# Kernel optimization log

Hardware: AMD Instinct MI355X
Metric: run time of the kernel (lower is better)

The kernel has to match this reference:

```python
import jax, jax.numpy as jnp
import numpy as np
from jax import lax

NPOINT = 1024
RADIUS = 0.2
NSAMPLE = 32
BN_EPS = 1e-5


def fps(xyz, npoint):
    """Deterministic farthest point sampling (start index 0). xyz: (B,N,3) -> (B,npoint) int32."""
    B, N, _ = xyz.shape

    def step(carry, _):
        distance, farthest = carry
        centroid = jnp.take_along_axis(xyz, farthest[:, None, None], axis=1)  # (B,1,3)
        d = jnp.sum((xyz - centroid) ** 2, axis=-1)  # (B,N)
        distance = jnp.minimum(distance, d)
        nxt = jnp.argmax(distance, axis=-1).astype(jnp.int32)
        return (distance, nxt), farthest

    init = (jnp.full((B, N), jnp.inf, dtype=xyz.dtype), jnp.zeros((B,), jnp.int32))
    _, idxs = lax.scan(step, init, None, length=npoint)  # (npoint, B)
    return jnp.transpose(idxs)  # (B, npoint)


def ball_query(radius, nsample, xyz, new_xyz):
    """Deterministic ball query: first nsample in-radius indices (sorted), padded with first hit.
    xyz: (B,N,3), new_xyz: (B,S,3) -> (B,S,nsample) int32."""
    B, N, _ = xyz.shape
    # squared distances via GEMM form to avoid (B,S,N,3) intermediate
    sqr = (jnp.sum(new_xyz ** 2, -1)[:, :, None]
           + jnp.sum(xyz ** 2, -1)[:, None, :]
           - 2.0 * jnp.einsum('bsd,bnd->bsn', new_xyz, xyz))  # (B,S,N)
    idx = jnp.where(sqr <= radius ** 2, jnp.arange(N, dtype=jnp.int32), N)
    idx = jnp.sort(idx, axis=-1)[:, :, :nsample]  # (B,S,K)
    first = idx[:, :, :1]
    first = jnp.where(first == N, 0, first)  # no point in radius -> index 0
    return jnp.where(idx == N, first, idx)


def setup_inputs() -> dict:
    key = jax.random.key(0)
    ks = jax.random.split(key, 8)
    B, N, Cin = 16, 4096, 64
    xyz = jax.random.uniform(ks[0], (B, N, 3), dtype=jnp.float32)
    points = jax.random.normal(ks[1], (B, Cin, N), dtype=jnp.float32)
    chans = [Cin + 3, 64, 64, 128]
    d = {"xyz": xyz, "points": points}
    for i in range(3):
        d[f"w{i}"] = jax.random.normal(ks[2 + i], (chans[i + 1], chans[i]), dtype=jnp.float32) / np.float32(np.sqrt(chans[i]))
        d[f"g{i}"] = jnp.ones((chans[i + 1],), dtype=jnp.float32)
        d[f"b{i}"] = jnp.zeros((chans[i + 1],), dtype=jnp.float32)
    return d


def _forward(xyz, points, params):
    B, N, _ = xyz.shape
    idx = fps(xyz, NPOINT)                                     # (B,S)
    new_xyz = jnp.take_along_axis(xyz, idx[:, :, None], axis=1)  # (B,S,3)
    gidx = ball_query(RADIUS, NSAMPLE, xyz, new_xyz)             # (B,S,K)
    gather = jax.vmap(lambda p, i: p[i])
    grouped_xyz = gather(xyz, gidx) - new_xyz[:, :, None, :]     # (B,S,K,3)
    grouped_pts = gather(jnp.transpose(points, (0, 2, 1)), gidx)  # (B,S,K,C)
    feats = jnp.concatenate([grouped_xyz, grouped_pts], axis=-1)  # (B,S,K,3+C)
    for (w, g, b) in params:
        feats = jnp.einsum('oc,bskc->bsko', w, feats)
        mean = jnp.mean(feats, axis=(0, 1, 2))
        var = jnp.var(feats, axis=(0, 1, 2))
        feats = (feats - mean) * (g * lax.rsqrt(var + BN_EPS)) + b  # BatchNorm (batch stats)
        feats = jax.nn.relu(feats)
    feats = jnp.max(feats, axis=2)               # (B,S,Cout) max-pool over neighbors
    return new_xyz, jnp.transpose(feats, (0, 2, 1))  # (B,Cout,S) channel-first like torch


def reference(xyz, points, w0, g0, b0, w1, g1, b1, w2, g2, b2):
    params = [(w0, g0, b0), (w1, g1, b1), (w2, g2, b2)]
    return _forward(xyz, points, params)
```

## Files before the change

### kernel.cpp

```cpp
#include <hip/hip_runtime.h>

#define DI static __device__ __forceinline__

typedef float v2f __attribute__((ext_vector_type(2)));
typedef __attribute__((ext_vector_type(8))) short bf16x8;
typedef __attribute__((ext_vector_type(4))) float f32x4;

DI unsigned short f2bf(float f) {
  unsigned int u = __float_as_uint(f);
  u = (u + 0x7fffu + ((u >> 16) & 1u)) >> 16;
  return (unsigned short)u;
}
DI float bf2f(unsigned short h) { return __uint_as_float(((unsigned int)h) << 16); }

DI v2f pk_sub(v2f a, v2f b) {
  v2f d;
  asm("v_pk_add_f32 %0, %1, %2 neg_lo:[0,1] neg_hi:[0,1]" : "=v"(d) : "v"(a), "v"(b));
  return d;
}
DI v2f pk_mul(v2f a, v2f b) {
  v2f d;
  asm("v_pk_mul_f32 %0, %1, %2" : "=v"(d) : "v"(a), "v"(b));
  return d;
}
DI v2f pk_add(v2f a, v2f b) {
  v2f d;
  asm("v_pk_add_f32 %0, %1, %2" : "=v"(d) : "v"(a), "v"(b));
  return d;
}

#define DPP_MAXU(v, ctrl)                                                      \
  {                                                                            \
    unsigned o_ = (unsigned)__builtin_amdgcn_update_dpp((int)(v), (int)(v),    \
                                                        (ctrl), 0xf, 0xf, false); \
    (v) = (o_ > (v)) ? o_ : (v);                                               \
  }
#define DPP_MINU(v, ctrl)                                                      \
  {                                                                            \
    unsigned o_ = (unsigned)__builtin_amdgcn_update_dpp((int)(v), (int)(v),    \
                                                        (ctrl), 0xf, 0xf, false); \
    (v) = (o_ < (v)) ? o_ : (v);                                               \
  }

__global__ __launch_bounds__(256) void fps_kernel(const float* __restrict__ xyz,
                                                  float* __restrict__ newxyz) {
  const int b = blockIdx.x;
  const int t = threadIdx.x;
  const int lane = t & 63, wid = t >> 6;
  const float* X = xyz + (size_t)b * 4096 * 3;
  __shared__ float XL[4096 * 3];
  __shared__ int FI[1024];
  __shared__ unsigned long long slot[2][4];
  for (int idx = t; idx < 12288; idx += 256) XL[idx] = X[idx];
  v2f px[8], py[8], pz[8], dist[8];
#pragma unroll
  for (int q = 0; q < 8; ++q) {
    int i0 = t + (q << 9);
    int i1 = i0 + 256;
    px[q] = (v2f){X[i0 * 3 + 0], X[i1 * 3 + 0]};
    py[q] = (v2f){X[i0 * 3 + 1], X[i1 * 3 + 1]};
    pz[q] = (v2f){X[i0 * 3 + 2], X[i1 * 3 + 2]};
    dist[q] = (v2f){3.402823466e38f, 3.402823466e38f};
  }
  __syncthreads();
  float cx = XL[0], cy = XL[1], cz = XL[2];
  int fi = 0;
  for (int s = 0; s < 1024; ++s) {
    if (t == 0) FI[s] = fi;
    float bv = -1.0f;
    unsigned int bi = 0;
    v2f cxv = (v2f){cx, cx}, cyv = (v2f){cy, cy}, czv = (v2f){cz, cz};
#pragma unroll
    for (int q = 0; q < 8; ++q) {
      v2f dx = pk_sub(px[q], cxv);
      v2f dy = pk_sub(py[q], cyv);
      v2f dz = pk_sub(pz[q], czv);
      v2f d = pk_add(pk_add(pk_mul(dx, dx), pk_mul(dy, dy)), pk_mul(dz, dz));
      float n0 = fminf(dist[q].x, d.x);
      float n1 = fminf(dist[q].y, d.y);
      dist[q].x = n0;
      dist[q].y = n1;
      bool c0 = (n0 > bv);
      bv = c0 ? n0 : bv;
      bi = c0 ? (unsigned)(t + (q << 9)) : bi;
      bool c1 = (n1 > bv);
      bv = c1 ? n1 : bv;
      bi = c1 ? (unsigned)(t + (q << 9) + 256) : bi;
    }
    unsigned vb = __float_as_uint(bv);
    unsigned m = vb;
    DPP_MAXU(m, 0x111);
    DPP_MAXU(m, 0x112);
    DPP_MAXU(m, 0x114);
    DPP_MAXU(m, 0x118);
    DPP_MAXU(m, 0x142);
    DPP_MAXU(m, 0x143);
    unsigned wmax = (unsigned)__builtin_amdgcn_readlane((int)m, 63);
    unsigned ik = (vb == wmax) ? bi : 0xFFFFFFFFu;
    DPP_MINU(ik, 0x111);
    DPP_MINU(ik, 0x112);
    DPP_MINU(ik, 0x114);
    DPP_MINU(ik, 0x118);
    DPP_MINU(ik, 0x142);
    DPP_MINU(ik, 0x143);
    unsigned widx = (unsigned)__builtin_amdgcn_readlane((int)ik, 63);
    const int p = s & 1;
    if (lane == 0)
      slot[p][wid] = ((unsigned long long)wmax << 32) | (unsigned long long)(~widx);
    __syncthreads();
    unsigned long long k0 = slot[p][0], k1 = slot[p][1];
    unsigned long long k2 = slot[p][2], k3 = slot[p][3];
    unsigned long long m01 = (k0 >= k1) ? k0 : k1;
    unsigned long long m23 = (k2 >= k3) ? k2 : k3;
    unsigned long long win = (m01 >= m23) ? m01 : m23;
    fi = (int)(~(unsigned int)win);
    cx = XL[fi * 3 + 0];
    cy = XL[fi * 3 + 1];
    cz = XL[fi * 3 + 2];
  }
  __syncthreads();
  float* out = newxyz + (size_t)b * 1024 * 3;
  for (int s2 = t; s2 < 1024; s2 += 256) {
    int f = FI[s2];
    out[s2 * 3 + 0] = XL[f * 3 + 0];
    out[s2 * 3 + 1] = XL[f * 3 + 1];
    out[s2 * 3 + 2] = XL[f * 3 + 2];
  }
}

__global__ __launch_bounds__(256) void p0_kernel(const float* __restrict__ points,
                                                 const float* __restrict__ w0,
                                                 float* __restrict__ P0) {
  const int b = blockIdx.x >> 6;
  const int n0 = (blockIdx.x & 63) << 6;
  const int t = threadIdx.x;
  __shared__ float W[64][64];
  for (int idx = t; idx < 4096; idx += 256) {
    int c = idx >> 6, o = idx & 63;
    W[c][o] = w0[o * 67 + 3 + c];
  }
  __syncthreads();
  const int i = t >> 4, j = t & 15;
  const float* Pb = points + (size_t)b * 64 * 4096 + n0 + 4 * i;
  float acc[4][4] = {};
  for (int c = 0; c < 64; ++c) {
    float4 xv = *(const float4*)(Pb + (size_t)c * 4096);
    float4 wv = *(const float4*)&W[c][4 * j];
    float xr[4] = {xv.x, xv.y, xv.z, xv.w};
    float wr[4] = {wv.x, wv.y, wv.z, wv.w};
#pragma unroll
    for (int rr = 0; rr < 4; ++rr)
#pragma unroll
      for (int oi = 0; oi < 4; ++oi) acc[rr][oi] = fmaf(xr[rr], wr[oi], acc[rr][oi]);
  }
#pragma unroll
  for (int rr = 0; rr < 4; ++rr) {
    float4 vv = make_float4(acc[rr][0], acc[rr][1], acc[rr][2], acc[rr][3]);
    *(float4*)(P0 + ((size_t)b * 4096 + n0 + 4 * i + rr) * 64 + 4 * j) = vv;
  }
}

__global__ __launch_bounds__(256) void ballquery_stats0_kernel(
    const float* __restrict__ xyz, const float* __restrict__ newxyz,
    const float* __restrict__ P0, const float* __restrict__ w0,
    int* __restrict__ gidx, float* __restrict__ partials0) {
  const int t = threadIdx.x;
  const int lane = t & 63, w = t >> 6;
  const int gid = blockIdx.x * 4 + w;
  const int b = gid >> 10;
  __shared__ int sel[4][32];
  __shared__ float red[4][128];
  const float* Xb = xyz + (size_t)b * 4096 * 3;
  const float cx = newxyz[(size_t)gid * 3 + 0];
  const float cy = newxyz[(size_t)gid * 3 + 1];
  const float cz = newxyz[(size_t)gid * 3 + 2];
  const float cs = __fadd_rn(__fadd_rn(__fmul_rn(cx, cx), __fmul_rn(cy, cy)), __fmul_rn(cz, cz));
  int cnt = 0, first = 0;
  bool found = false;
  for (int base = 0; base < 4096; base += 64) {
    int i = base + lane;
    float x = Xb[i * 3 + 0], y = Xb[i * 3 + 1], z = Xb[i * 3 + 2];
    float xs = __fadd_rn(__fadd_rn(__fmul_rn(x, x), __fmul_rn(y, y)), __fmul_rn(z, z));
    float dot = fmaf(cz, z, fmaf(cy, y, __fmul_rn(cx, x)));
    float sqr = __fsub_rn(__fadd_rn(cs, xs), __fmul_rn(2.0f, dot));
    bool ok = sqr <= 0.04f;
    unsigned long long mask = __ballot(ok);
    if (!found && mask != 0ull) { first = base + __builtin_ctzll(mask); found = true; }
    int pre = __popcll(mask & ((1ull << lane) - 1ull));
    int pos = cnt + pre;
    if (ok && pos < 32) sel[w][pos] = i;
    cnt += (int)__popcll(mask);
    if (cnt >= 32) break;
  }
  if (cnt < 32) {
    int pad = found ? first : 0;
    for (int p = cnt + lane; p < 32; p += 64) sel[w][p] = pad;
  }
  __syncthreads();
  if (lane < 32) gidx[(size_t)gid * 32 + lane] = sel[w][lane];
  const int c = lane;
  float wx = w0[c * 67 + 0], wy = w0[c * 67 + 1], wz = w0[c * 67 + 2];
  float ssum = 0.f, ssq = 0.f;
  const float* P0b = P0 + (size_t)b * 4096 * 64;
  for (int k = 0; k < 32; ++k) {
    int g = sel[w][k];
    float gx = Xb[g * 3 + 0] - cx, gy = Xb[g * 3 + 1] - cy, gz = Xb[g * 3 + 2] - cz;
    float a0 = fmaf(wx, gx, fmaf(wy, gy, fmaf(wz, gz, P0b[(size_t)g * 64 + c])));
    ssum += a0;
    ssq = fmaf(a0, a0, ssq);
  }
  red[w][c] = ssum;
  red[w][c + 64] = ssq;
  __syncthreads();
  if (t < 128) {
    float acc = red[0][t] + red[1][t] + red[2][t] + red[3][t];
    partials0[(size_t)t * 4096 + blockIdx.x] = acc;
  }
}

__global__ __launch_bounds__(256) void finalize_kernel(
    const float* __restrict__ partials, int C, int nblk,
    const float* __restrict__ gamma, const float* __restrict__ beta,
    float* __restrict__ scale, float* __restrict__ shift) {
  const int c = blockIdx.x, t = threadIdx.x;
  double s1 = 0.0, s2 = 0.0;
  for (int k = t; k < nblk; k += 256) {
    s1 += (double)partials[(size_t)c * nblk + k];
    s2 += (double)partials[(size_t)(C + c) * nblk + k];
  }
  __shared__ double r1[256], r2[256];
  r1[t] = s1;
  r2[t] = s2;
  __syncthreads();
  for (int off = 128; off > 0; off >>= 1) {
    if (t < off) { r1[t] += r1[t + off]; r2[t] += r2[t + off]; }
    __syncthreads();
  }
  if (t == 0) {
    const double M = 524288.0;
    double mean = r1[0] / M;
    double var = r2[0] / M - mean * mean;
    if (var < 0.0) var = 0.0;
    float sc = gamma[c] * (float)(1.0 / sqrt(var + 1e-5));
    scale[c] = sc;
    shift[c] = beta[c] - (float)mean * sc;
  }
}

__global__ __launch_bounds__(256) void p2_kernel(
    const float* __restrict__ xyz, const float* __restrict__ newxyz,
    const float* __restrict__ P0, const int* __restrict__ gidx,
    const float* __restrict__ w0, const float* __restrict__ w1,
    const float* __restrict__ sc0g, const float* __restrict__ sh0g,
    unsigned short* __restrict__ act1, float* __restrict__ partials1) {
  __shared__ unsigned short W1T[64 * 72];
  __shared__ unsigned short A[64 * 72];
  __shared__ float S1r[4][68], S2r[4][68];
  __shared__ float w0x[64], w0y[64], w0z[64], sc0[64], sh0[64];
  const int t = threadIdx.x;
  const int lane = t & 63, w = t >> 6;
  const int quad = lane >> 4, l15 = lane & 15;
  for (int idx = t; idx < 4096; idx += 256) {
    int o = idx >> 6, c = idx & 63;
    W1T[o * 72 + c] = f2bf(w1[o * 64 + c]);
  }
  if (t < 64) {
    w0x[t] = w0[t * 67 + 0];
    w0y[t] = w0[t * 67 + 1];
    w0z[t] = w0[t * 67 + 2];
    sc0[t] = sc0g[t];
    sh0[t] = sh0g[t];
  }
  __syncthreads();
  const int rl = t >> 2, cq = t & 3;
  float ssum[4] = {}, ssq[4] = {};
  for (int tile = 0; tile < 8; ++tile) {
    const int rowbase = (blockIdx.x * 8 + tile) << 6;
    {
      int r = rowbase + rl;
      int b = r >> 15, s = (r >> 5) & 1023;
      int g = gidx[r];
      const float* Pt = xyz + ((size_t)b * 4096 + g) * 3;
      const float* Ct = newxyz + ((size_t)b * 1024 + s) * 3;
      float dx = Pt[0] - Ct[0], dy = Pt[1] - Ct[1], dz = Pt[2] - Ct[2];
      const float4* p4 = (const float4*)(P0 + ((size_t)b * 4096 + g) * 64 + cq * 16);
      float4 a0 = p4[0], a1 = p4[1], a2 = p4[2], a3 = p4[3];
      float pv[16] = {a0.x, a0.y, a0.z, a0.w, a1.x, a1.y, a1.z, a1.w,
                      a2.x, a2.y, a2.z, a2.w, a3.x, a3.y, a3.z, a3.w};
      unsigned pk[8];
#pragma unroll
      for (int q = 0; q < 8; ++q) {
        int c0 = cq * 16 + 2 * q, c1 = c0 + 1;
        float aa = fmaf(w0x[c0], dx, fmaf(w0y[c0], dy, fmaf(w0z[c0], dz, pv[2 * q])));
        float bb = fmaf(w0x[c1], dx, fmaf(w0y[c1], dy, fmaf(w0z[c1], dz, pv[2 * q + 1])));
        float r0 = fmaxf(0.f, fmaf(aa, sc0[c0], sh0[c0]));
        float r1 = fmaxf(0.f, fmaf(bb, sc0[c1], sh0[c1]));
        pk[q] = (unsigned)f2bf(r0) | ((unsigned)f2bf(r1) << 16);
      }
      uint4* dst = (uint4*)&A[rl * 72 + cq * 16];
      dst[0] = make_uint4(pk[0], pk[1], pk[2], pk[3]);
      dst[1] = make_uint4(pk[4], pk[5], pk[6], pk[7]);
    }
    __syncthreads();
    const unsigned short* Arow = &A[(w * 16 + l15) * 72 + quad * 8];
    bf16x8 a0 = *(const bf16x8*)(Arow);
    bf16x8 a1 = *(const bf16x8*)(Arow + 32);
#pragma unroll
    for (int nt = 0; nt < 4; ++nt) {
      const unsigned short* Brow = &W1T[(nt * 16 + l15) * 72 + quad * 8];
      bf16x8 b0 = *(const bf16x8*)(Brow);
      bf16x8 b1 = *(const bf16x8*)(Brow + 32);
      f32x4 c0 = {0.f, 0.f, 0.f, 0.f};
      c0 = __builtin_amdgcn_mfma_f32_16x16x32_bf16(a0, b0, c0, 0, 0, 0);
      c0 = __builtin_amdgcn_mfma_f32_16x16x32_bf16(a1, b1, c0, 0, 0, 0);
      size_t rbase = (size_t)rowbase + w * 16 + quad * 4;
      int o = nt * 16 + l15;
#pragma unroll
      for (int reg = 0; reg < 4; ++reg) {
        float y = c0[reg];
        ssum[nt] += y;
        ssq[nt] = fmaf(y, y, ssq[nt]);
        act1[(rbase + reg) * 64 + o] = f2bf(y);
      }
    }
    __syncthreads();
  }
#pragma unroll
  for (int nt = 0; nt < 4; ++nt) {
    float s1 = ssum[nt];
    s1 += __shfl_xor(s1, 16, 64);
    s1 += __shfl_xor(s1, 32, 64);
    float s2 = ssq[nt];
    s2 += __shfl_xor(s2, 16, 64);
    s2 += __shfl_xor(s2, 32, 64);
    if (quad == 0) {
      S1r[w][nt * 16 + l15] = s1;
      S2r[w][nt * 16 + l15] = s2;
    }
  }
  __syncthreads();
  if (t < 64) {
    int o = t;
    float s1 = S1r[0][o] + S1r[1][o] + S1r[2][o] + S1r[3][o];
    float s2 = S2r[0][o] + S2r[1][o] + S2r[2][o] + S2r[3][o];
    partials1[(size_t)o * 1024 + blockIdx.x] = s1;
    partials1[(size_t)(64 + o) * 1024 + blockIdx.x] = s2;
  }
}

__global__ __launch_bounds__(256) void p3_kernel(
    const unsigned short* __restrict__ act1, const float* __restrict__ w2,
    const float* __restrict__ sc1g, const float* __restrict__ sh1g,
    float* __restrict__ partials2, float* __restrict__ gmx,
    float* __restrict__ gmn) {
  __shared__ unsigned short W2T[128 * 72];
  __shared__ unsigned short A[64 * 72];
  __shared__ float Mred[4][132], Nred[4][132];
  __shared__ float S1r[4][132], S2r[4][132];
  __shared__ float sc1[64], sh1[64];
  const int t = threadIdx.x;
  const int lane = t & 63, w = t >> 6;
  const int quad = lane >> 4, l15 = lane & 15;
  for (int idx = t; idx < 8192; idx += 256) {
    int o = idx >> 6, c = idx & 63;
    W2T[o * 72 + c] = f2bf(w2[o * 64 + c]);
  }
  if (t < 64) { sc1[t] = sc1g[t]; sh1[t] = sh1g[t]; }
  __syncthreads();
  const int rl = t >> 2, cq = t & 3;
  float ssum[8] = {}, ssq[8] = {};
  for (int tile = 0; tile < 8; ++tile) {
    const int rowbase = (blockIdx.x * 8 + tile) << 6;
    {
      size_t r = (size_t)rowbase + rl;
      const uint4* pr = (const uint4*)(act1 + r * 64 + cq * 16);
      uint4 aa = pr[0], bb = pr[1];
      unsigned int uu[8] = {aa.x, aa.y, aa.z, aa.w, bb.x, bb.y, bb.z, bb.w};
      unsigned int pk[8];
#pragma unroll
      for (int q = 0; q < 8; ++q) {
        int c = cq * 16 + 2 * q;
        float v0 = bf2f((unsigned short)(uu[q] & 0xffffu));
        float v1 = bf2f((unsigned short)(uu[q] >> 16));
        float r0 = fmaxf(0.f, fmaf(v0, sc1[c], sh1[c]));
        float r1 = fmaxf(0.f, fmaf(v1, sc1[c + 1], sh1[c + 1]));
        pk[q] = (unsigned)f2bf(r0) | ((unsigned)f2bf(r1) << 16);
      }
      uint4* dst = (uint4*)&A[rl * 72 + cq * 16];
      dst[0] = make_uint4(pk[0], pk[1], pk[2], pk[3]);
      dst[1] = make_uint4(pk[4], pk[5], pk[6], pk[7]);
    }
    __syncthreads();
    const unsigned short* Arow = &A[(w * 16 + l15) * 72 + quad * 8];
    bf16x8 a0 = *(const bf16x8*)(Arow);
    bf16x8 a1 = *(const bf16x8*)(Arow + 32);
    f32x4 acc[8];
#pragma unroll
    for (int nt = 0; nt < 8; ++nt) {
      const unsigned short* Brow = &W2T[(nt * 16 + l15) * 72 + quad * 8];
      bf16x8 b0 = *(const bf16x8*)(Brow);
      bf16x8 b1 = *(const bf16x8*)(Brow + 32);
      f32x4 c0 = {0.f, 0.f, 0.f, 0.f};
      c0 = __builtin_amdgcn_mfma_f32_16x16x32_bf16(a0, b0, c0, 0, 0, 0);
      c0 = __builtin_amdgcn_mfma_f32_16x16x32_bf16(a1, b1, c0, 0, 0, 0);
      acc[nt] = c0;
    }
#pragma unroll
    for (int nt = 0; nt < 8; ++nt) {
      float y0 = acc[nt][0], y1 = acc[nt][1], y2 = acc[nt][2], y3 = acc[nt][3];
      ssum[nt] += ((y0 + y1) + (y2 + y3));
      ssq[nt] = fmaf(y0, y0, ssq[nt]);
      ssq[nt] = fmaf(y1, y1, ssq[nt]);
      ssq[nt] = fmaf(y2, y2, ssq[nt]);
      ssq[nt] = fmaf(y3, y3, ssq[nt]);
      float mx = fmaxf(fmaxf(y0, y1), fmaxf(y2, y3));
      float mn = fminf(fminf(y0, y1), fminf(y2, y3));
      mx = fmaxf(mx, __shfl_xor(mx, 16, 64));
      mx = fmaxf(mx, __shfl_xor(mx, 32, 64));
      mn = fminf(mn, __shfl_xor(mn, 16, 64));
      mn = fminf(mn, __shfl_xor(mn, 32, 64));
      if (quad == 0) {
        Mred[w][nt * 16 + l15] = mx;
        Nred[w][nt * 16 + l15] = mn;
      }
    }
    __syncthreads();
    {
      int o = t & 127, g = t >> 7;
      float mx = fmaxf(Mred[2 * g][o], Mred[2 * g + 1][o]);
      float mn = fminf(Nred[2 * g][o], Nred[2 * g + 1][o]);
      int bb2 = rowbase >> 15;
      int ss2 = ((rowbase >> 5) & 1023) + g;
      size_t oidx = ((size_t)bb2 * 128 + o) * 1024 + ss2;
      gmx[oidx] = mx;
      gmn[oidx] = mn;
    }
    __syncthreads();
  }
#pragma unroll
  for (int nt = 0; nt < 8; ++nt) {
    float s1 = ssum[nt];
    s1 += __shfl_xor(s1, 16, 64);
    s1 += __shfl_xor(s1, 32, 64);
    float s2 = ssq[nt];
    s2 += __shfl_xor(s2, 16, 64);
    s2 += __shfl_xor(s2, 32, 64);
    if (quad == 0) {
      S1r[w][nt * 16 + l15] = s1;
      S2r[w][nt * 16 + l15] = s2;
    }
  }
  __syncthreads();
  if (t < 128) {
    int o = t;
    float s1 = S1r[0][o] + S1r[1][o] + S1r[2][o] + S1r[3][o];
    float s2 = S2r[0][o] + S2r[1][o] + S2r[2][o] + S2r[3][o];
    partials2[(size_t)o * 1024 + blockIdx.x] = s1;
    partials2[(size_t)(128 + o) * 1024 + blockIdx.x] = s2;
  }
}

__global__ __launch_bounds__(256) void p4f_kernel(
    const float* __restrict__ gmx, const float* __restrict__ gmn,
    const float* __restrict__ sc2g, const float* __restrict__ sh2g,
    float* __restrict__ feats) {
  const int bo = blockIdx.x >> 2;
  const int s = ((blockIdx.x & 3) << 8) + threadIdx.x;
  const int o = bo & 127;
  const float sc = sc2g[o], sh = sh2g[o];
  size_t idx = (size_t)bo * 1024 + s;
  float v = (sc >= 0.f) ? gmx[idx] : gmn[idx];
  feats[idx] = fmaxf(0.f, fmaf(v, sc, sh));
}

extern "C" void kernel_launch(void* const* d_in, const int* in_sizes, int n_in,
                              void* d_out, int out_size, void* d_ws, size_t ws_size,
                              hipStream_t stream) {
  const float* xyz = (const float*)d_in[0];
  const float* points = (const float*)d_in[1];
  const float* w0 = (const float*)d_in[2];
  const float* g0 = (const float*)d_in[3];
  const float* b0 = (const float*)d_in[4];
  const float* w1 = (const float*)d_in[5];
  const float* g1 = (const float*)d_in[6];
  const float* b1 = (const float*)d_in[7];
  const float* w2 = (const float*)d_in[8];
  const float* g2 = (const float*)d_in[9];
  const float* b2 = (const float*)d_in[10];

  float* out = (float*)d_out;
  float* newxyz = out;
  float* feats = out + 49152;

  char* ws = (char*)d_ws;
  float* P0 = (float*)ws;
  float* gmx = (float*)ws;
  float* gmn = (float*)(ws + (size_t)(8u << 20));
  int* gidx = (int*)(ws + (size_t)(16u << 20));
  unsigned short* act1 = (unsigned short*)(ws + (size_t)(18u << 20));
  float* partials0 = (float*)(ws + (size_t)(82u << 20));
  float* partials1 = (float*)(ws + (size_t)(84u << 20));
  float* partials2 = (float*)(ws + (size_t)(85u << 20));
  float* sc0 = (float*)(ws + (size_t)(86u << 20));
  float* sh0 = sc0 + 128;
  float* sc1 = sc0 + 256;
  float* sh1 = sc0 + 384;
  float* sc2 = sc0 + 512;
  float* sh2 = sc0 + 640;

  fps_kernel<<<16, 256, 0, stream>>>(xyz, newxyz);
  p0_kernel<<<1024, 256, 0, stream>>>(points, w0, P0);
  ballquery_stats0_kernel<<<4096, 256, 0, stream>>>(xyz, newxyz, P0, w0, gidx, partials0);
  finalize_kernel<<<64, 256, 0, stream>>>(partials0, 64, 4096, g0, b0, sc0, sh0);
  p2_kernel<<<1024, 256, 0, stream>>>(xyz, newxyz, P0, gidx, w0, w1, sc0, sh0, act1, partials1);
  finalize_kernel<<<64, 256, 0, stream>>>(partials1, 64, 1024, g1, b1, sc1, sh1);
  p3_kernel<<<1024, 256, 0, stream>>>(act1, w2, sc1, sh1, partials2, gmx, gmn);
  finalize_kernel<<<128, 256, 0, stream>>>(partials2, 128, 1024, g2, b2, sc2, sh2);
  p4f_kernel<<<8192, 256, 0, stream>>>(gmx, gmn, sc2, sh2, feats);
}
```

Measured before the change: 938.8 us.

## Stage act1 stores through LDS, transpose max/min layout, use compiler packed math in FPS

In p2, MFMA outputs are first written into an LDS tile and then copied to act1 as coalesced 16-byte row stores, replacing scattered 2-byte global stores. p3 now writes the per-centroid max/min in (B,S,O) order so its stores are contiguous. p4f is rewritten to read those tiles into LDS and transpose them before writing channel-first output, using 1024 blocks instead of 8192. The FPS inner loop swaps inline-asm packed ops for vector expressions with FP contraction disabled, which should keep the numerics the same and give the compiler more freedom to schedule.

```diff
diff --git a/kernel.cpp b/kernel.cpp
--- a/kernel.cpp
+++ b/kernel.cpp
@@ -12,22 +12,6 @@
   return (unsigned short)u;
 }
 DI float bf2f(unsigned short h) { return __uint_as_float(((unsigned int)h) << 16); }
-
-DI v2f pk_sub(v2f a, v2f b) {
-  v2f d;
-  asm("v_pk_add_f32 %0, %1, %2 neg_lo:[0,1] neg_hi:[0,1]" : "=v"(d) : "v"(a), "v"(b));
-  return d;
-}
-DI v2f pk_mul(v2f a, v2f b) {
-  v2f d;
-  asm("v_pk_mul_f32 %0, %1, %2" : "=v"(d) : "v"(a), "v"(b));
-  return d;
-}
-DI v2f pk_add(v2f a, v2f b) {
-  v2f d;
-  asm("v_pk_add_f32 %0, %1, %2" : "=v"(d) : "v"(a), "v"(b));
-  return d;
-}
 
 #define DPP_MAXU(v, ctrl)                                                      \
   {                                                                            \
@@ -72,14 +56,20 @@
     v2f cxv = (v2f){cx, cx}, cyv = (v2f){cy, cy}, czv = (v2f){cz, cz};
 #pragma unroll
     for (int q = 0; q < 8; ++q) {
-      v2f dx = pk_sub(px[q], cxv);
-      v2f dy = pk_sub(py[q], cyv);
-      v2f dz = pk_sub(pz[q], czv);
-      v2f d = pk_add(pk_add(pk_mul(dx, dx), pk_mul(dy, dy)), pk_mul(dz, dz));
-      float n0 = fminf(dist[q].x, d.x);
-      float n1 = fminf(dist[q].y, d.y);
-      dist[q].x = n0;
-      dist[q].y = n1;
+#pragma clang fp contract(off)
+      v2f dx = px[q] - cxv;
+      v2f dy = py[q] - cyv;
+      v2f dz = pz[q] - czv;
+      v2f d = (dx * dx + dy * dy) + dz * dz;
+#if __has_builtin(__builtin_elementwise_min)
+      v2f nd = __builtin_elementwise_min(dist[q], d);
+#else
+      v2f nd;
+      nd.x = fminf(dist[q].x, d.x);
+      nd.y = fminf(dist[q].y, d.y);
+#endif
+      dist[q] = nd;
+      float n0 = nd.x, n1 = nd.y;
       bool c0 = (n0 > bv);
       bv = c0 ? n0 : bv;
       bi = c0 ? (unsigned)(t + (q << 9)) : bi;
@@ -255,6 +245,7 @@
     unsigned short* __restrict__ act1, float* __restrict__ partials1) {
   __shared__ unsigned short W1T[64 * 72];
   __shared__ unsigned short A[64 * 72];
+  __shared__ unsigned short Cs[64 * 72];
   __shared__ float S1r[4][68], S2r[4][68];
   __shared__ float w0x[64], w0y[64], w0z[64], sc0[64], sh0[64];
   const int t = threadIdx.x;
@@ -313,17 +304,24 @@
       f32x4 c0 = {0.f, 0.f, 0.f, 0.f};
       c0 = __builtin_amdgcn_mfma_f32_16x16x32_bf16(a0, b0, c0, 0, 0, 0);
       c0 = __builtin_amdgcn_mfma_f32_16x16x32_bf16(a1, b1, c0, 0, 0, 0);
-      size_t rbase = (size_t)rowbase + w * 16 + quad * 4;
       int o = nt * 16 + l15;
+      int rloc = w * 16 + quad * 4;
 #pragma unroll
       for (int reg = 0; reg < 4; ++reg) {
         float y = c0[reg];
         ssum[nt] += y;
         ssq[nt] = fmaf(y, y, ssq[nt]);
-        act1[(rbase + reg) * 64 + o] = f2bf(y);
+        Cs[(rloc + reg) * 72 + o] = f2bf(y);
       }
     }
     __syncthreads();
+    {
+      const uint4* src = (const uint4*)&Cs[rl * 72 + cq * 16];
+      uint4 v0 = src[0], v1 = src[1];
+      uint4* dst = (uint4*)(act1 + ((size_t)rowbase + rl) * 64 + cq * 16);
+      dst[0] = v0;
+      dst[1] = v1;
+    }
   }
 #pragma unroll
   for (int nt = 0; nt < 4; ++nt) {
@@ -431,7 +429,7 @@
       float mn = fminf(Nred[2 * g][o], Nred[2 * g + 1][o]);
       int bb2 = rowbase >> 15;
       int ss2 = ((rowbase >> 5) & 1023) + g;
-      size_t oidx = ((size_t)bb2 * 128 + o) * 1024 + ss2;
+      size_t oidx = ((size_t)bb2 * 1024 + ss2) * 128 + o;
       gmx[oidx] = mx;
       gmn[oidx] = mn;
     }
@@ -464,13 +462,28 @@
     const float* __restrict__ gmx, const float* __restrict__ gmn,
     const float* __restrict__ sc2g, const float* __restrict__ sh2g,
     float* __restrict__ feats) {
-  const int bo = blockIdx.x >> 2;
-  const int s = ((blockIdx.x & 3) << 8) + threadIdx.x;
-  const int o = bo & 127;
-  const float sc = sc2g[o], sh = sh2g[o];
-  size_t idx = (size_t)bo * 1024 + s;
-  float v = (sc >= 0.f) ? gmx[idx] : gmn[idx];
-  feats[idx] = fmaxf(0.f, fmaf(v, sc, sh));
+  __shared__ float MX[16 * 130], MN[16 * 130];
+  const int t = threadIdx.x;
+  const int bb = blockIdx.x >> 6;
+  const int s0 = (blockIdx.x & 63) << 4;
+#pragma unroll
+  for (int k = 0; k < 8; ++k) {
+    int idx = k * 256 + t;
+    int s = idx >> 7, o = idx & 127;
+    size_t g = ((size_t)bb * 1024 + s0 + s) * 128 + o;
+    MX[s * 130 + o] = gmx[g];
+    MN[s * 130 + o] = gmn[g];
+  }
+  __syncthreads();
+  const int oo = t >> 1, shf = t & 1;
+  const float sc = sc2g[oo], sh = sh2g[oo];
+  float* dst = feats + ((size_t)bb * 128 + oo) * 1024 + s0 + shf * 8;
+#pragma unroll
+  for (int k = 0; k < 8; ++k) {
+    int s = shf * 8 + k;
+    float v = (sc >= 0.f) ? MX[s * 130 + oo] : MN[s * 130 + oo];
+    dst[k] = fmaxf(0.f, fmaf(v, sc, sh));
+  }
 }
 
 extern "C" void kernel_launch(void* const* d_in, const int* in_sizes, int n_in,
@@ -516,5 +529,5 @@
   finalize_kernel<<<64, 256, 0, stream>>>(partials1, 64, 1024, g1, b1, sc1, sh1);
   p3_kernel<<<1024, 256, 0, stream>>>(act1, w2, sc1, sh1, partials2, gmx, gmn);
   finalize_kernel<<<128, 256, 0, stream>>>(partials2, 128, 1024, g2, b2, sc2, sh2);
-  p4f_kernel<<<8192, 256, 0, stream>>>(gmx, gmn, sc2, sh2, feats);
-}
+  p4f_kernel<<<1024, 256, 0, stream>>>(gmx, gmn, sc2, sh2, feats);
+}
```

Result: faster. 874.2 us (-6.9%).
